# Kernel tuning notes

Measured on AMD Instinct MI355X. Metric: run time of the kernel, lower is better.

The kernel has to match this reference:

```python
import jax, jax.numpy as jnp
import numpy as np


def _ste_round(r):
    # straight-through round
    return r + jax.lax.stop_gradient(jnp.round(r) - r)


def quant_sym(x, s, qn, qp):
    # symmetric LSQ-style fake-quant: clamp(round(x/s)) * s
    r = jnp.clip(x / s, qn, qp)
    return _ste_round(r) * s


def quant_asym(x, s, beta, qn, qp):
    # asymmetric fake-quant with learnable zero-point beta
    r = jnp.clip((x - beta) / s, qn, qp)
    return _ste_round(r) * s + beta


def quant_weight_statsq(w, n_bits=8):
    # statsq: per-output-channel scale from weight statistics
    qp = 2 ** (n_bits - 1) - 1          # 127
    qn = -(2 ** (n_bits - 1))           # -128
    s = 2.0 * jnp.mean(jnp.abs(w), axis=1, keepdims=True) / jnp.sqrt(float(qp))
    return quant_sym(w, s, qn, qp)


def setup_inputs() -> dict:
    key = jax.random.key(0)
    ks = jax.random.split(key, 8)
    B, N, C, H = 4, 4096, 1024, 4096
    x = jax.random.normal(ks[0], (B, N, C), dtype=jnp.float32)
    w1 = jax.random.normal(ks[1], (H, C), dtype=jnp.float32) * (1.0 / np.sqrt(C))
    b1 = jax.random.normal(ks[2], (H,), dtype=jnp.float32) * 0.01
    w2 = jax.random.normal(ks[3], (C, H), dtype=jnp.float32) * (1.0 / np.sqrt(H))
    b2 = jax.random.normal(ks[4], (C,), dtype=jnp.float32) * 0.01
    # learnable LSQ activation scales (per input channel), kept positive
    s_a1 = 0.05 + 0.05 * jax.random.uniform(ks[5], (C,), dtype=jnp.float32)
    s_a2 = 0.02 + 0.02 * jax.random.uniform(ks[6], (H,), dtype=jnp.float32)
    beta2 = jnp.zeros((H,), dtype=jnp.float32)
    return {"x": x, "w1": w1, "b1": b1, "w2": w2, "b2": b2,
            "s_a1": s_a1, "s_a2": s_a2, "beta2": beta2}


def reference(x, w1, b1, w2, b2, s_a1, s_a2, beta2):
    # fc1: symmetric 8-bit LSQ on input, statsq 8-bit on weight
    xq = quant_sym(x, s_a1, -128, 127)
    wq1 = quant_weight_statsq(w1)
    h = jnp.einsum('bnc,hc->bnh', xq, wq1) + b1
    h = jax.nn.gelu(h, approximate=False)  # nn.GELU default (exact erf)
    # drop1 = identity in eval
    # fc2: asymmetric 8-bit LSQ on (non-negative-skewed) activations
    hq = quant_asym(h, s_a2, beta2, 0, 255)
    wq2 = quant_weight_statsq(w2)
    out = jnp.einsum('bnh,ch->bnc', hq, wq2) + b2
    # drop2 = identity in eval
    return out
```

## Files before the change

### kernel.cpp

```cpp
#include <hip/hip_runtime.h>
#include <cstdint>
#include <cstddef>

typedef __attribute__((ext_vector_type(8))) short short8;
typedef __attribute__((ext_vector_type(4))) float f32x4;
typedef __attribute__((ext_vector_type(4))) unsigned short ushort4_t;

__device__ __forceinline__ unsigned short f2bf(float f) {
  unsigned u = __float_as_uint(f);
  u += 0x7FFFu + ((u >> 16) & 1u);
  return (unsigned short)(u >> 16);
}

__device__ __forceinline__ void gload_lds16(const void* g, void* lds) {
  __builtin_amdgcn_global_load_lds((const __attribute__((address_space(1))) void*)g,
                                   (__attribute__((address_space(3))) void*)lds,
                                   16, 0, 0);
}

__device__ __forceinline__ float erf_fast(float v) {
  float x = fabsf(v);
  float t = __builtin_amdgcn_rcpf(fmaf(0.3275911f, x, 1.0f));
  float p = fmaf(1.061405429f, t, -1.453152027f);
  p = fmaf(p, t, 1.421413741f);
  p = fmaf(p, t, -0.284496736f);
  p = fmaf(p, t, 0.254829592f);
  p = p * t;
  float e = fmaf(-p, __expf(-x * x), 1.0f);
  unsigned s = __float_as_uint(v) & 0x80000000u;
  return __uint_as_float(__float_as_uint(e) | s);
}

__global__ void quant_x_kernel(const float4* __restrict__ x, const float* __restrict__ s_a1,
                               ushort4_t* __restrict__ xq, int n4, int c4mask) {
  const int stride = gridDim.x * blockDim.x;
  for (int i = blockIdx.x * blockDim.x + threadIdx.x; i < n4; i += stride) {
    float4 v = x[i];
    int c = (i & c4mask) << 2;
    float vv[4] = {v.x, v.y, v.z, v.w};
    ushort4_t o;
#pragma unroll
    for (int j = 0; j < 4; ++j) {
      float s = s_a1[c + j];
      float r = vv[j] / s;
      r = fminf(fmaxf(r, -128.f), 127.f);
      o[j] = f2bf(rintf(r) * s);
    }
    xq[i] = o;
  }
}

__global__ void quant_w_kernel(const float* __restrict__ w, unsigned short* __restrict__ wq,
                               int cols) {
  const int row = blockIdx.x;
  const float* wr = w + (size_t)row * cols;
  float part = 0.f;
  for (int j = threadIdx.x; j < cols; j += blockDim.x) part += fabsf(wr[j]);
#pragma unroll
  for (int o = 32; o > 0; o >>= 1) part += __shfl_down(part, o, 64);
  __shared__ float wsum[4];
  if ((threadIdx.x & 63) == 0) wsum[threadIdx.x >> 6] = part;
  __syncthreads();
  float mean = (wsum[0] + wsum[1] + wsum[2] + wsum[3]) / (float)cols;
  float s = 2.f * mean / sqrtf(127.f);
  unsigned short* wqr = wq + (size_t)row * cols;
  for (int j = threadIdx.x; j < cols; j += blockDim.x) {
    float r = wr[j] / s;
    r = fminf(fmaxf(r, -128.f), 127.f);
    wqr[j] = f2bf(rintf(r) * s);
  }
}

#define BAR() __builtin_amdgcn_s_barrier()
#define SB() __builtin_amdgcn_sched_barrier(0)
#define LGKM(n) { asm volatile("s_waitcnt lgkmcnt(" #n ")" ::: "memory"); SB(); }
#define VMC0() { asm volatile("s_waitcnt vmcnt(0)" ::: "memory"); SB(); }
#define PRIO1() __builtin_amdgcn_s_setprio(1)
#define PRIO0() __builtin_amdgcn_s_setprio(0)

#define STG(gbase, ldsbuf, h, kt) { \
  _Pragma("unroll") for (int i_ = 0; i_ < 2; ++i_) { \
    const int rb_ = (h) * 128 + (w * 2 + i_) * 8; \
    gload_lds16((gbase) + (size_t)rb_ * K + (size_t)(kt) * 64, (void*)((ldsbuf) + rb_ * 64)); } }

#define LDA_(dst, buf, mh) { \
  _Pragma("unroll") for (int mi_ = 0; mi_ < 4; ++mi_) { \
    dst[mi_][0] = *(const short8*)((buf) + aBase + (mh) * 4096 + mi_ * 1024 + ck0); \
    dst[mi_][1] = *(const short8*)((buf) + aBase + (mh) * 4096 + mi_ * 1024 + ck1); } }

#define LDB_(dst, buf, nh) { \
  _Pragma("unroll") for (int ni_ = 0; ni_ < 2; ++ni_) { \
    dst[ni_][0] = *(const short8*)((buf) + bBase + (nh) * 2048 + ni_ * 1024 + ck0); \
    dst[ni_][1] = *(const short8*)((buf) + bBase + (nh) * 2048 + ni_ * 1024 + ck1); } }

#define MMQ(aR, bR, mh, nh) { \
  _Pragma("unroll") for (int kk_ = 0; kk_ < 2; ++kk_) \
  _Pragma("unroll") for (int mi_ = 0; mi_ < 4; ++mi_) \
  _Pragma("unroll") for (int ni_ = 0; ni_ < 2; ++ni_) \
    acc[(mh) * 4 + mi_][(nh) * 2 + ni_] = __builtin_amdgcn_mfma_f32_16x16x32_bf16( \
        aR[mi_][kk_], bR[ni_][kk_], acc[(mh) * 4 + mi_][(nh) * 2 + ni_], 0, 0, 0); }

template <int EPI>
__global__ __launch_bounds__(512, 2) void gemm_bt_pl(
    const unsigned short* __restrict__ A, const unsigned short* __restrict__ B,
    const float* __restrict__ bias, const float* __restrict__ s2,
    const float* __restrict__ beta, unsigned short* __restrict__ Cq,
    float* __restrict__ Cf, int N, int K)
{
  __shared__ __align__(16) unsigned short As0[256 * 64];
  __shared__ __align__(16) unsigned short As1[256 * 64];
  __shared__ __align__(16) unsigned short Bs0[256 * 64];
  __shared__ __align__(16) unsigned short Bs1[256 * 64];

  const int tid = threadIdx.x;
  const int w = tid >> 6, ll = tid & 63;
  const int wr = w >> 2, wc = w & 3;

  const int nwg = gridDim.x * gridDim.y;
  const int bid = blockIdx.x + gridDim.x * blockIdx.y;
  const int cpx = nwg >> 3;
  const int swz = (bid & 7) * cpx + (bid >> 3);
  const int gy = gridDim.y;
  const int bx = swz / gy, by = swz - bx * gy;
  const long bm = (long)bx * 256;
  const long bn = (long)by * 256;

  const int srow = ll >> 3;
  const int scol = ((ll & 7) ^ srow) << 3;
  const unsigned short* Agl = A + ((size_t)bm + srow) * K + scol;
  const unsigned short* Bgl = B + ((size_t)bn + srow) * K + scol;

  const int lhi = ll >> 4, llo = ll & 15, l7 = ll & 7;
  const int ck0 = ((0 * 4 + lhi) ^ l7) * 8;
  const int ck1 = ((1 * 4 + lhi) ^ l7) * 8;
  const int aBase = (wr * 128 + llo) * 64;
  const int bBase = (wc * 64 + llo) * 64;

  f32x4 acc[8][4] = {};
  short8 a0[4][2], a1[4][2], b0[2][2], b1[2][2];

  const int nkt = K >> 6;

  STG(Agl, As0, 0, 0); STG(Agl, As0, 1, 0);
  STG(Bgl, Bs0, 0, 0); STG(Bgl, Bs0, 1, 0);
  STG(Agl, As1, 0, 1); STG(Agl, As1, 1, 1);
  STG(Bgl, Bs1, 0, 1); STG(Bgl, Bs1, 1, 1);
  asm volatile("s_waitcnt vmcnt(8)" ::: "memory"); SB();
  BAR();
  LDA_(a0, As0, 0);
  LDB_(b0, Bs0, 0);

  for (int t = 0; t < nkt; ++t) {
    unsigned short* Asb = (t & 1) ? As1 : As0;
    unsigned short* Bsb = (t & 1) ? Bs1 : Bs0;
    unsigned short* Asn = (t & 1) ? As0 : As1;
    unsigned short* Bsn = (t & 1) ? Bs0 : Bs1;
    const bool i1 = (t + 1 < nkt), i2 = (t + 2 < nkt);

    LDB_(b1, Bsb, 1);
    LGKM(4);
    PRIO1(); MMQ(a0, b0, 0, 0); PRIO0();
    LDA_(a1, Asb, 1);
    LGKM(8);
    PRIO1(); MMQ(a0, b1, 0, 1); PRIO0();
    LGKM(0);
    PRIO1(); MMQ(a1, b0, 1, 0); PRIO0();
    VMC0();
    BAR();
    if (i2) {
      STG(Agl, Asb, 0, t + 2); STG(Agl, Asb, 1, t + 2);
      STG(Bgl, Bsb, 0, t + 2); STG(Bgl, Bsb, 1, t + 2);
    }
    if (i1) {
      LDA_(a0, Asn, 0);
      LDB_(b0, Bsn, 0);
    }
    PRIO1(); MMQ(a1, b1, 1, 1); PRIO0();
  }

  const int lr = lhi;
  const int lc = llo;
#pragma unroll
  for (int NI = 0; NI < 4; ++NI) {
    const long col = bn + wc * 64 + NI * 16 + lc;
    const float bv = bias[col];
    float sv = 1.f, bev = 0.f, inv = 1.f;
    if (EPI == 0) { sv = s2[col]; bev = beta[col]; inv = 1.0f / sv; }
#pragma unroll
    for (int MI = 0; MI < 8; ++MI) {
#pragma unroll
      for (int r = 0; r < 4; ++r) {
        const size_t rowg = (size_t)(bm + wr * 128 + MI * 16 + lr * 4 + r);
        float v = acc[MI][NI][r] + bv;
        if (EPI == 0) {
          float g = 0.5f * v * (1.f + erf_fast(v * 0.70710678118654752f));
          float rr = (g - bev) * inv;
          rr = fminf(fmaxf(rr, 0.f), 255.f);
          Cq[rowg * N + col] = f2bf(fmaf(rintf(rr), sv, bev));
        } else {
          Cf[rowg * N + col] = v;
        }
      }
    }
  }
}

extern "C" void kernel_launch(void* const* d_in, const int* in_sizes, int n_in,
                              void* d_out, int out_size, void* d_ws, size_t ws_size,
                              hipStream_t stream) {
  const float* x     = (const float*)d_in[0];
  const float* w1    = (const float*)d_in[1];
  const float* b1    = (const float*)d_in[2];
  const float* w2    = (const float*)d_in[3];
  const float* b2    = (const float*)d_in[4];
  const float* s_a1  = (const float*)d_in[5];
  const float* s_a2  = (const float*)d_in[6];
  const float* beta2 = (const float*)d_in[7];
  float* out = (float*)d_out;

  const int C = 1024, H = 4096;
  const int M = in_sizes[0] / C;

  unsigned short* xq  = (unsigned short*)d_ws;
  unsigned short* wq1 = xq  + (size_t)M * C;
  unsigned short* wq2 = wq1 + (size_t)H * C;
  unsigned short* hq  = wq2 + (size_t)C * H;

  quant_x_kernel<<<2048, 256, 0, stream>>>((const float4*)x, s_a1, (ushort4_t*)xq,
                                           M * C / 4, C / 4 - 1);
  quant_w_kernel<<<H, 256, 0, stream>>>(w1, wq1, C);
  quant_w_kernel<<<C, 256, 0, stream>>>(w2, wq2, H);

  dim3 g1(M / 256, H / 256);
  gemm_bt_pl<0><<<g1, 512, 0, stream>>>(xq, wq1, b1, s_a2, beta2, hq, nullptr, H, C);
  dim3 g2(M / 256, C / 256);
  gemm_bt_pl<1><<<g2, 512, 0, stream>>>(hq, wq2, b2, nullptr, nullptr, nullptr, out, C, H);
}
```

Baseline: 356.7 us.

## Restructure GEMM main loop into four barrier-separated phases with interleaved loads

Rewrites the GEMM K-loop as four phases. Each phase issues an LDS fragment read and one quarter of the next-next tile's global-to-LDS copy, then hits a barrier and runs one MFMA quadrant. Warp B columns are remapped so each warp owns two 32-column stripes split across the tile halves, with a matching change to the epilogue column mapping. The aim is to spread global loads evenly and keep the waves in lock-step, like ping-pong schedules. The cost is many more barriers and full lgkmcnt(0) waits per iteration, which can serialize LDS latency with MFMA work.

```diff
diff --git a/kernel.cpp b/kernel.cpp
--- a/kernel.cpp
+++ b/kernel.cpp
@@ -73,8 +73,7 @@
 
 #define BAR() __builtin_amdgcn_s_barrier()
 #define SB() __builtin_amdgcn_sched_barrier(0)
-#define LGKM(n) { asm volatile("s_waitcnt lgkmcnt(" #n ")" ::: "memory"); SB(); }
-#define VMC0() { asm volatile("s_waitcnt vmcnt(0)" ::: "memory"); SB(); }
+#define LGKM0() { asm volatile("s_waitcnt lgkmcnt(0)" ::: "memory"); SB(); }
 #define PRIO1() __builtin_amdgcn_s_setprio(1)
 #define PRIO0() __builtin_amdgcn_s_setprio(0)
 
@@ -88,10 +87,10 @@
     dst[mi_][0] = *(const short8*)((buf) + aBase + (mh) * 4096 + mi_ * 1024 + ck0); \
     dst[mi_][1] = *(const short8*)((buf) + aBase + (mh) * 4096 + mi_ * 1024 + ck1); } }
 
-#define LDB_(dst, buf, nh) { \
+#define LDBX(dst, buf, base) { \
   _Pragma("unroll") for (int ni_ = 0; ni_ < 2; ++ni_) { \
-    dst[ni_][0] = *(const short8*)((buf) + bBase + (nh) * 2048 + ni_ * 1024 + ck0); \
-    dst[ni_][1] = *(const short8*)((buf) + bBase + (nh) * 2048 + ni_ * 1024 + ck1); } }
+    dst[ni_][0] = *(const short8*)((buf) + (base) + ni_ * 1024 + ck0); \
+    dst[ni_][1] = *(const short8*)((buf) + (base) + ni_ * 1024 + ck1); } }
 
 #define MMQ(aR, bR, mh, nh) { \
   _Pragma("unroll") for (int kk_ = 0; kk_ < 2; ++kk_) \
@@ -101,7 +100,7 @@
         aR[mi_][kk_], bR[ni_][kk_], acc[(mh) * 4 + mi_][(nh) * 2 + ni_], 0, 0, 0); }
 
 template <int EPI>
-__global__ __launch_bounds__(512, 2) void gemm_bt_pl(
+__global__ __launch_bounds__(512, 2) void gemm_bt_m2(
     const unsigned short* __restrict__ A, const unsigned short* __restrict__ B,
     const float* __restrict__ bias, const float* __restrict__ s2,
     const float* __restrict__ beta, unsigned short* __restrict__ Cq,
@@ -134,55 +133,60 @@
   const int ck0 = ((0 * 4 + lhi) ^ l7) * 8;
   const int ck1 = ((1 * 4 + lhi) ^ l7) * 8;
   const int aBase = (wr * 128 + llo) * 64;
-  const int bBase = (wc * 64 + llo) * 64;
+  const int bBase0 = (wc * 32 + llo) * 64;
+  const int bBase1 = (128 + wc * 32 + llo) * 64;
 
   f32x4 acc[8][4] = {};
   short8 a0[4][2], a1[4][2], b0[2][2], b1[2][2];
 
   const int nkt = K >> 6;
 
-  STG(Agl, As0, 0, 0); STG(Agl, As0, 1, 0);
-  STG(Bgl, Bs0, 0, 0); STG(Bgl, Bs0, 1, 0);
-  STG(Agl, As1, 0, 1); STG(Agl, As1, 1, 1);
-  STG(Bgl, Bs1, 0, 1); STG(Bgl, Bs1, 1, 1);
+  STG(Bgl, Bs0, 0, 0); STG(Agl, As0, 0, 0); STG(Agl, As0, 1, 0); STG(Bgl, Bs0, 1, 0);
+  STG(Bgl, Bs1, 0, 1); STG(Agl, As1, 0, 1); STG(Agl, As1, 1, 1); STG(Bgl, Bs1, 1, 1);
   asm volatile("s_waitcnt vmcnt(8)" ::: "memory"); SB();
   BAR();
-  LDA_(a0, As0, 0);
-  LDB_(b0, Bs0, 0);
+  LDBX(b0, Bs0, bBase0);
+  LGKM0();
+  BAR();
 
   for (int t = 0; t < nkt; ++t) {
     unsigned short* Asb = (t & 1) ? As1 : As0;
     unsigned short* Bsb = (t & 1) ? Bs1 : Bs0;
-    unsigned short* Asn = (t & 1) ? As0 : As1;
     unsigned short* Bsn = (t & 1) ? Bs0 : Bs1;
     const bool i1 = (t + 1 < nkt), i2 = (t + 2 < nkt);
 
-    LDB_(b1, Bsb, 1);
-    LGKM(4);
+    LDA_(a0, Asb, 0);
+    if (i2) STG(Bgl, Bsb, 0, t + 2);
+    BAR(); LGKM0();
     PRIO1(); MMQ(a0, b0, 0, 0); PRIO0();
+    BAR();
+
     LDA_(a1, Asb, 1);
-    LGKM(8);
+    if (i2) STG(Agl, Asb, 0, t + 2);
+    BAR(); LGKM0();
+    PRIO1(); MMQ(a1, b0, 1, 0); PRIO0();
+    BAR();
+
+    LDBX(b1, Bsb, bBase1);
+    if (i2) STG(Agl, Asb, 1, t + 2);
+    BAR(); LGKM0();
+    PRIO1(); MMQ(a1, b1, 1, 1); PRIO0();
+    BAR();
+
+    if (i1) LDBX(b0, Bsn, bBase0);
+    if (i2) STG(Bgl, Bsb, 1, t + 2);
+    if (i2)      { asm volatile("s_waitcnt vmcnt(6)" ::: "memory"); SB(); }
+    else if (i1) { asm volatile("s_waitcnt vmcnt(0)" ::: "memory"); SB(); }
+    BAR(); LGKM0();
     PRIO1(); MMQ(a0, b1, 0, 1); PRIO0();
-    LGKM(0);
-    PRIO1(); MMQ(a1, b0, 1, 0); PRIO0();
-    VMC0();
-    BAR();
-    if (i2) {
-      STG(Agl, Asb, 0, t + 2); STG(Agl, Asb, 1, t + 2);
-      STG(Bgl, Bsb, 0, t + 2); STG(Bgl, Bsb, 1, t + 2);
-    }
-    if (i1) {
-      LDA_(a0, Asn, 0);
-      LDB_(b0, Bsn, 0);
-    }
-    PRIO1(); MMQ(a1, b1, 1, 1); PRIO0();
+    BAR();
   }
 
   const int lr = lhi;
   const int lc = llo;
 #pragma unroll
   for (int NI = 0; NI < 4; ++NI) {
-    const long col = bn + wc * 64 + NI * 16 + lc;
+    const long col = bn + wc * 32 + ((NI >= 2) ? 128 : 0) + (NI & 1) * 16 + lc;
     const float bv = bias[col];
     float sv = 1.f, bev = 0.f, inv = 1.f;
     if (EPI == 0) { sv = s2[col]; bev = beta[col]; inv = 1.0f / sv; }
@@ -232,7 +236,7 @@
   quant_w_kernel<<<C, 256, 0, stream>>>(w2, wq2, H);
 
   dim3 g1(M / 256, H / 256);
-  gemm_bt_pl<0><<<g1, 512, 0, stream>>>(xq, wq1, b1, s_a2, beta2, hq, nullptr, H, C);
+  gemm_bt_m2<0><<<g1, 512, 0, stream>>>(xq, wq1, b1, s_a2, beta2, hq, nullptr, H, C);
   dim3 g2(M / 256, C / 256);
-  gemm_bt_pl<1><<<g2, 512, 0, stream>>>(hq, wq2, b2, nullptr, nullptr, nullptr, out, C, H);
-}
+  gemm_bt_m2<1><<<g2, 512, 0, stream>>>(hq, wq2, b2, nullptr, nullptr, nullptr, out, C, H);
+}
```

Result: slower. 370.4 us (+3.9%).
